# Optimization experiments

Hardware: AMD Instinct MI355X
Metric: run time of the kernel (lower is better)

The kernel has to match this reference:

```python
import jax, jax.numpy as jnp
import numpy as np

B, T, D, H = 64, 512, 1024, 1024


def setup_inputs() -> dict:
    key = jax.random.key(0)
    ks = jax.random.split(key, 8)
    s_in = 1.0 / np.sqrt(D).astype(np.float32)
    s_h = 1.0 / np.sqrt(H).astype(np.float32)
    return {
        "x": jax.random.normal(ks[0], (B, T, D), jnp.float32),
        "lengths": jax.random.randint(ks[1], (B,), 0, T),
        "k0": jax.random.normal(ks[2], (D, 3 * H), jnp.float32) * s_in,
        "rk0": jax.random.normal(ks[3], (H, 3 * H), jnp.float32) * s_h,
        "b0": jax.random.normal(ks[4], (2, 3 * H), jnp.float32) * 0.02,
        "k1": jax.random.normal(ks[5], (H, 3 * H), jnp.float32) * s_h,
        "rk1": jax.random.normal(ks[6], (H, 3 * H), jnp.float32) * s_h,
        "b1": jax.random.normal(ks[7], (2, 3 * H), jnp.float32) * 0.02,
    }


def _gru_step(h, xt, k, rk, b):
    # Keras GRUCell, reset_after=True (v2): separate input/recurrent biases.
    mx = xt @ k + b[0]          # [B, 3H]
    mh = h @ rk + b[1]          # [B, 3H]
    xz, xr, xh = jnp.split(mx, 3, axis=-1)
    hz, hr, hh = jnp.split(mh, 3, axis=-1)
    z = jax.nn.sigmoid(xz + hz)
    r = jax.nn.sigmoid(xr + hr)
    cand = jnp.tanh(xh + r * hh)
    return z * h + (1.0 - z) * cand


def reference(x, lengths, k0, rk0, b0, k1, rk1, b1):
    Bb, Tt, _ = x.shape
    mask = jnp.arange(Tt)[None, :] < lengths[:, None]   # [B, T]

    def step(carry, inp):
        h0, h1 = carry
        xt, mt = inp                                    # xt [B,D], mt [B]
        nh0 = _gru_step(h0, xt, k0, rk0, b0)
        nh1 = _gru_step(h1, nh0, k1, rk1, b1)
        m = mt[:, None]
        h0 = jnp.where(m, nh0, h0)                      # masked steps carry state
        h1 = jnp.where(m, nh1, h1)
        return (h0, h1), h1                             # output = top-layer state

    h_init = (jnp.zeros((Bb, k1.shape[1] // 3), x.dtype),
              jnp.zeros((Bb, k1.shape[1] // 3), x.dtype))
    _, ys = jax.lax.scan(step, h_init, (x.transpose(1, 0, 2), mask.T))
    return ys.transpose(1, 0, 2)                        # [B, T, H]
```

## Files before the change

kernel.cpp:

```cpp
#include <hip/hip_runtime.h>
#include <cstdint>


typedef unsigned short u16;
typedef __bf16 bf16x8 __attribute__((ext_vector_type(8)));
typedef float f32x4 __attribute__((ext_vector_type(4)));

#define B_   64
#define T_   512
#define D_   1024
#define H_   1024
#define N3_  3072
#define TC_  32
#define NCH_ 16
#define MROWS_ (B_ * TC_)

#define MFMA(a, b, c) __builtin_amdgcn_mfma_f32_16x16x32_bf16((a), (b), (c), 0, 0, 0)

static __device__ __forceinline__ u16 f2bf(float x) {
  unsigned u = __float_as_uint(x);
  u += 0x7FFFu + ((u >> 16) & 1u);
  return (u16)(u >> 16);
}
static __device__ __forceinline__ float bf2f(u16 s) {
  return __uint_as_float(((unsigned)s) << 16);
}

__global__ void init_ws(u16* s0h, u16* s0l, u16* s1h, u16* s1l,
                        unsigned* bars) {
  int i = blockIdx.x * blockDim.x + threadIdx.x;
  if (i < B_ * H_) { s0h[i] = 0; s0l[i] = 0; s1h[i] = 0; s1l[i] = 0; }
  if (i < 2 * NCH_ * 256) bars[i] = 0;
}

__global__ void split_x_chunk(const float* __restrict__ x, int t0,
                              u16* __restrict__ hi, u16* __restrict__ lo) {
  int i = blockIdx.x * blockDim.x + threadIdx.x;
  int m = i >> 8;
  int c = i & 255;
  int tl = m >> 6;
  int b = m & 63;
  float4 v = ((const float4*)x)[((size_t)b * T_ + t0 + tl) * 256 + c];
  u16 h0 = f2bf(v.x), h1 = f2bf(v.y), h2 = f2bf(v.z), h3 = f2bf(v.w);
  u16 g0 = f2bf(v.x - bf2f(h0)), g1 = f2bf(v.y - bf2f(h1));
  u16 g2 = f2bf(v.z - bf2f(h2)), g3 = f2bf(v.w - bf2f(h3));
  uint2 ph, pl;
  ph.x = (unsigned)h0 | ((unsigned)h1 << 16);
  ph.y = (unsigned)h2 | ((unsigned)h3 << 16);
  pl.x = (unsigned)g0 | ((unsigned)g1 << 16);
  pl.y = (unsigned)g2 | ((unsigned)g3 << 16);
  *(uint2*)(hi + (size_t)i * 4) = ph;
  *(uint2*)(lo + (size_t)i * 4) = pl;
}

__global__ void transpose_split(const float* __restrict__ src, u16* __restrict__ dhi,
                                u16* __restrict__ dlo) {
  __shared__ float tile[32][33];
  const int tx = threadIdx.x, ty = threadIdx.y;
  const int n0 = blockIdx.x * 32, k0 = blockIdx.y * 32;
  #pragma unroll
  for (int i = 0; i < 4; ++i)
    tile[ty + 8 * i][tx] = src[(size_t)(k0 + ty + 8 * i) * N3_ + n0 + tx];
  __syncthreads();
  #pragma unroll
  for (int i = 0; i < 4; ++i) {
    float v = tile[tx][ty + 8 * i];
    size_t o = (size_t)(n0 + ty + 8 * i) * 1024 + k0 + tx;
    u16 h = f2bf(v);
    dhi[o] = h;
    dlo[o] = f2bf(v - bf2f(h));
  }
}

__global__ __launch_bounds__(256, 1) void gemm_bf16x3(
    const u16* __restrict__ Ahi, const u16* __restrict__ Alo,
    const u16* __restrict__ Bhi, const u16* __restrict__ Blo,
    const float* __restrict__ bias, float* __restrict__ C) {
  __shared__ u16 lds[4 * 128 * 64];
  u16* ldsAh = lds;
  u16* ldsAl = lds + 128 * 64;
  u16* ldsBh = lds + 2 * 128 * 64;
  u16* ldsBl = lds + 3 * 128 * 64;

  const int tid = threadIdx.x;
  const int wave = tid >> 6, lane = tid & 63;
  const int l15 = lane & 15, l4 = lane >> 4;
  const int wm = wave >> 1, wn = wave & 1;
  const int m0 = blockIdx.y * 128, n0 = blockIdx.x * 128;

  f32x4 acc[4][4];
  f32x4 zero = {0.f, 0.f, 0.f, 0.f};
  #pragma unroll
  for (int i = 0; i < 4; ++i)
    #pragma unroll
    for (int j = 0; j < 4; ++j) acc[i][j] = zero;

  for (int kt = 0; kt < 16; ++kt) {
    #pragma unroll
    for (int q = 0; q < 4; ++q) {
      int chunk = q * 256 + tid;
      int row = chunk >> 3, cc = chunk & 7;
      int sc = cc ^ (row & 7);
      size_t ga = (size_t)(m0 + row) * 1024 + kt * 64 + cc * 8;
      size_t gb = (size_t)(n0 + row) * 1024 + kt * 64 + cc * 8;
      int lo_ = row * 64 + sc * 8;
      *(uint4*)(ldsAh + lo_) = *(const uint4*)(Ahi + ga);
      *(uint4*)(ldsAl + lo_) = *(const uint4*)(Alo + ga);
      *(uint4*)(ldsBh + lo_) = *(const uint4*)(Bhi + gb);
      *(uint4*)(ldsBl + lo_) = *(const uint4*)(Blo + gb);
    }
    __syncthreads();
    #pragma unroll
    for (int kk = 0; kk < 2; ++kk) {
      bf16x8 ah[4], al[4], bh[4], bl[4];
      #pragma unroll
      for (int mt = 0; mt < 4; ++mt) {
        int row = wm * 64 + mt * 16 + l15;
        int off = row * 64 + ((4 * kk + l4) ^ (row & 7)) * 8;
        ah[mt] = *(const bf16x8*)(ldsAh + off);
        al[mt] = *(const bf16x8*)(ldsAl + off);
      }
      #pragma unroll
      for (int nt = 0; nt < 4; ++nt) {
        int row = wn * 64 + nt * 16 + l15;
        int off = row * 64 + ((4 * kk + l4) ^ (row & 7)) * 8;
        bh[nt] = *(const bf16x8*)(ldsBh + off);
        bl[nt] = *(const bf16x8*)(ldsBl + off);
      }
      #pragma unroll
      for (int mt = 0; mt < 4; ++mt)
        #pragma unroll
        for (int nt = 0; nt < 4; ++nt) {
          acc[mt][nt] = MFMA(ah[mt], bh[nt], acc[mt][nt]);
          acc[mt][nt] = MFMA(ah[mt], bl[nt], acc[mt][nt]);
          acc[mt][nt] = MFMA(al[mt], bh[nt], acc[mt][nt]);
        }
    }
    __syncthreads();
  }
  #pragma unroll
  for (int nt = 0; nt < 4; ++nt) {
    int col = n0 + wn * 64 + nt * 16 + l15;
    float bv = bias[col];
    #pragma unroll
    for (int mt = 0; mt < 4; ++mt) {
      int rowb = m0 + wm * 64 + mt * 16 + 4 * l4;
      #pragma unroll
      for (int r = 0; r < 4; ++r)
        C[(size_t)(rowb + r) * N3_ + col] = acc[mt][nt][r] + bv;
    }
  }
}

__global__ __launch_bounds__(256, 1) void gru_rec_v2(
    const float* __restrict__ mx, const u16* __restrict__ wTh,
    const u16* __restrict__ wTl, const float* __restrict__ bias,
    const int* __restrict__ lengths, u16* __restrict__ Sh, u16* __restrict__ Sl,
    u16* __restrict__ Hh, u16* __restrict__ Hl, float* __restrict__ outF32,
    unsigned* __restrict__ bars, int t0) {
  __shared__ __align__(16) char lds[77824];
  char* ldsAh = lds;
  char* ldsAl = lds + 32768;
  char* ldsRed = lds + 65536;

  const int bid = blockIdx.x;
  const int colgrp = bid & 63, mtile = bid >> 6;
  const int tid = threadIdx.x;
  const int wave = tid >> 6, lane = tid & 63;
  const int l15 = lane & 15, l4 = lane >> 4;
  const int ccol = colgrp * 16 + l15;
  unsigned* bar = bars + mtile * 64;

  const int kbase = wave * 256 + 8 * l4;
  bf16x8 Wh[3][8], Wl[3][8];
  #pragma unroll
  for (int g = 0; g < 3; ++g) {
    const size_t wrow = ((size_t)(g * 1024 + ccol)) * 1024 + kbase;
    #pragma unroll
    for (int ks = 0; ks < 8; ++ks) {
      Wh[g][ks] = *(const bf16x8*)(wTh + wrow + ks * 32);
      Wl[g][ks] = *(const bf16x8*)(wTl + wrow + ks * 32);
    }
  }

  const float bz = bias[ccol], br = bias[1024 + ccol], bh = bias[2048 + ccol];
  const int brow = mtile * 16 + 4 * l4;
  int lens[4];
  #pragma unroll
  for (int r = 0; r < 4; ++r) lens[r] = lengths[brow + r];
  const int grow0 = mtile * 16;

  #pragma unroll 1
  for (int tl = 0; tl < TC_; ++tl) {
    const u16* srcH = (tl == 0) ? Sh : (Hh + (size_t)(tl - 1) * B_ * H_);
    const u16* srcL = (tl == 0) ? Sl : (Hl + (size_t)(tl - 1) * B_ * H_);

    float pxz[4], pxr[4], pxh[4], phold[4];
    if (wave == 0) {
      #pragma unroll
      for (int r = 0; r < 4; ++r) {
        int b = brow + r;
        size_t mrow = ((size_t)tl * B_ + b) * N3_;
        pxz[r] = mx[mrow + ccol];
        pxr[r] = mx[mrow + 1024 + ccol];
        pxh[r] = mx[mrow + 2048 + ccol];
        size_t poff = (size_t)b * H_ + ccol;
        phold[r] = bf2f(srcH[poff]) + bf2f(srcL[poff]);
      }
    }

    #pragma unroll
    for (int i = 0; i < 8; ++i) {
      int c = i * 256 + tid;
      int row = c >> 7, k16 = c & 127;
      int dso = row * 2048 + ((k16 * 16) ^ ((row & 7) << 4));
      size_t go = (size_t)(grow0 + row) * H_ + k16 * 8;
      *(uint4*)(ldsAh + dso) = *(const uint4*)(srcH + go);
      *(uint4*)(ldsAl + dso) = *(const uint4*)(srcL + go);
    }
    __syncthreads();

    f32x4 a0 = {0.f, 0.f, 0.f, 0.f};
    f32x4 a1 = a0, a2 = a0;
    #pragma unroll
    for (int ks = 0; ks < 8; ++ks) {
      int k16 = wave * 32 + ks * 4 + l4;
      int dso = l15 * 2048 + ((k16 * 16) ^ ((l15 & 7) << 4));
      bf16x8 ah = *(const bf16x8*)(ldsAh + dso);
      bf16x8 al = *(const bf16x8*)(ldsAl + dso);
      a0 = MFMA(ah, Wh[0][ks], a0); a0 = MFMA(ah, Wl[0][ks], a0); a0 = MFMA(al, Wh[0][ks], a0);
      a1 = MFMA(ah, Wh[1][ks], a1); a1 = MFMA(ah, Wl[1][ks], a1); a1 = MFMA(al, Wh[1][ks], a1);
      a2 = MFMA(ah, Wh[2][ks], a2); a2 = MFMA(ah, Wl[2][ks], a2); a2 = MFMA(al, Wh[2][ks], a2);
    }

    if (wave != 0) {
      int rb = (wave - 1) * 3072;
      *(f32x4*)(ldsRed + rb + 0 * 1024 + lane * 16) = a0;
      *(f32x4*)(ldsRed + rb + 1 * 1024 + lane * 16) = a1;
      *(f32x4*)(ldsRed + rb + 2 * 1024 + lane * 16) = a2;
    }
    __syncthreads();

    if (wave == 0) {
      #pragma unroll
      for (int w = 1; w < 4; ++w) {
        int rb = (w - 1) * 3072;
        a0 += *(const f32x4*)(ldsRed + rb + 0 * 1024 + lane * 16);
        a1 += *(const f32x4*)(ldsRed + rb + 1 * 1024 + lane * 16);
        a2 += *(const f32x4*)(ldsRed + rb + 2 * 1024 + lane * 16);
      }
      const int t = t0 + tl;
      #pragma unroll
      for (int r = 0; r < 4; ++r) {
        int b = brow + r;
        float hz = a0[r] + bz, hr = a1[r] + br, hhv = a2[r] + bh;
        float z  = 1.f / (1.f + __expf(-(pxz[r] + hz)));
        float rg = 1.f / (1.f + __expf(-(pxr[r] + hr)));
        float ct = pxh[r] + rg * hhv;
        float e2 = __expf(2.f * ct);
        float cand = 1.f - 2.f / (e2 + 1.f);
        float hnew = (t < lens[r]) ? (z * phold[r] + (1.f - z) * cand) : phold[r];
        size_t crow = ((size_t)tl * B_ + b) * H_ + ccol;
        u16 nhi = f2bf(hnew);
        u16 nlo = f2bf(hnew - bf2f(nhi));
        Hh[crow] = nhi; Hl[crow] = nlo;
        if (outF32) outF32[((size_t)b * T_ + t) * H_ + ccol] = hnew;
        if (tl == TC_ - 1) {
          size_t poff = (size_t)b * H_ + ccol;
          Sh[poff] = nhi; Sl[poff] = nlo;
        }
      }
    }

    if (tl != TC_ - 1) {
      if (tid == 0) {
        __hip_atomic_fetch_add(bar, 1u, __ATOMIC_RELEASE, __HIP_MEMORY_SCOPE_AGENT);
        unsigned tgt = 64u * (unsigned)(tl + 1);
        while (__hip_atomic_load(bar, __ATOMIC_RELAXED, __HIP_MEMORY_SCOPE_AGENT) < tgt)
          __builtin_amdgcn_s_sleep(8);
        __threadfence();
      }
      __syncthreads();
    }
  }
}

extern "C" void kernel_launch(void* const* d_in, const int* in_sizes, int n_in,
                              void* d_out, int out_size, void* d_ws, size_t ws_size,
                              hipStream_t stream) {
  (void)in_sizes; (void)n_in; (void)out_size; (void)ws_size;
  const float* x      = (const float*)d_in[0];
  const int* lengths  = (const int*)d_in[1];
  const float* k0     = (const float*)d_in[2];
  const float* rk0    = (const float*)d_in[3];
  const float* b0     = (const float*)d_in[4];
  const float* k1     = (const float*)d_in[5];
  const float* rk1    = (const float*)d_in[6];
  const float* b1     = (const float*)d_in[7];
  float* out = (float*)d_out;
  char* ws = (char*)d_ws;

  const size_t WB = (size_t)N3_ * 1024 * 2;
  const size_t XB = (size_t)MROWS_ * 1024 * 2;
  size_t off = 0;
  u16* k0Th  = (u16*)(ws + off); off += WB;
  u16* k0Tl  = (u16*)(ws + off); off += WB;
  u16* rk0Th = (u16*)(ws + off); off += WB;
  u16* rk0Tl = (u16*)(ws + off); off += WB;
  u16* k1Th  = (u16*)(ws + off); off += WB;
  u16* k1Tl  = (u16*)(ws + off); off += WB;
  u16* rk1Th = (u16*)(ws + off); off += WB;
  u16* rk1Tl = (u16*)(ws + off); off += WB;
  u16* XCh   = (u16*)(ws + off); off += XB;
  u16* XCl   = (u16*)(ws + off); off += XB;
  float* MX  = (float*)(ws + off); off += (size_t)MROWS_ * N3_ * 4;
  u16* H0h   = (u16*)(ws + off); off += XB;
  u16* H0l   = (u16*)(ws + off); off += XB;
  u16* H1h   = (u16*)(ws + off); off += XB;
  u16* H1l   = (u16*)(ws + off); off += XB;
  u16* S0h   = (u16*)(ws + off); off += (size_t)B_ * H_ * 2;
  u16* S0l   = (u16*)(ws + off); off += (size_t)B_ * H_ * 2;
  u16* S1h   = (u16*)(ws + off); off += (size_t)B_ * H_ * 2;
  u16* S1l   = (u16*)(ws + off); off += (size_t)B_ * H_ * 2;
  unsigned* bars = (unsigned*)(ws + off); off += (size_t)2 * NCH_ * 256 * 4;

  init_ws<<<256, 256, 0, stream>>>(S0h, S0l, S1h, S1l, bars);

  dim3 tb(32, 8), tg(96, 32);
  transpose_split<<<tg, tb, 0, stream>>>(k0,  k0Th,  k0Tl);
  transpose_split<<<tg, tb, 0, stream>>>(rk0, rk0Th, rk0Tl);
  transpose_split<<<tg, tb, 0, stream>>>(k1,  k1Th,  k1Tl);
  transpose_split<<<tg, tb, 0, stream>>>(rk1, rk1Th, rk1Tl);

  for (int c = 0; c < NCH_; ++c) {
    int t0 = c * TC_;
    split_x_chunk<<<2048, 256, 0, stream>>>(x, t0, XCh, XCl);
    gemm_bf16x3<<<dim3(24, 16), 256, 0, stream>>>(XCh, XCl, k0Th, k0Tl, b0, MX);
    gru_rec_v2<<<256, 256, 0, stream>>>(MX, rk0Th, rk0Tl, b0 + N3_, lengths,
                                        S0h, S0l, H0h, H0l, nullptr,
                                        bars + (size_t)c * 256, t0);
    gemm_bf16x3<<<dim3(24, 16), 256, 0, stream>>>(H0h, H0l, k1Th, k1Tl, b1, MX);
    gru_rec_v2<<<256, 256, 0, stream>>>(MX, rk1Th, rk1Tl, b1 + N3_, lengths,
                                        S1h, S1l, H1h, H1l, out,
                                        bars + (size_t)(NCH_ + c) * 256, t0);
  }
}
```

Measured before the change: 15.47 ms.

## Pack hidden state hi/lo into u32 and lighten cross-block barrier

```diff
diff --git a/kernel.cpp b/kernel.cpp
--- a/kernel.cpp
+++ b/kernel.cpp
@@ -3,6 +3,8 @@
 
 
 typedef unsigned short u16;
+typedef unsigned int u32;
+typedef unsigned long long u64;
 typedef __bf16 bf16x8 __attribute__((ext_vector_type(8)));
 typedef float f32x4 __attribute__((ext_vector_type(4)));
 
@@ -26,10 +28,9 @@
   return __uint_as_float(((unsigned)s) << 16);
 }
 
-__global__ void init_ws(u16* s0h, u16* s0l, u16* s1h, u16* s1l,
-                        unsigned* bars) {
+__global__ void init_ws(u32* s0, u32* s1, unsigned* bars) {
   int i = blockIdx.x * blockDim.x + threadIdx.x;
-  if (i < B_ * H_) { s0h[i] = 0; s0l[i] = 0; s1h[i] = 0; s1l[i] = 0; }
+  if (i < B_ * H_) { s0[i] = 0; s1[i] = 0; }
   if (i < 2 * NCH_ * 256) bars[i] = 0;
 }
 
@@ -152,15 +153,15 @@
   }
 }
 
-__global__ __launch_bounds__(256, 1) void gru_rec_v2(
+__global__ __launch_bounds__(256, 1) void gru_rec_v3(
     const float* __restrict__ mx, const u16* __restrict__ wTh,
     const u16* __restrict__ wTl, const float* __restrict__ bias,
-    const int* __restrict__ lengths, u16* __restrict__ Sh, u16* __restrict__ Sl,
+    const int* __restrict__ lengths,
+    u32* __restrict__ Spk, u32* __restrict__ Hpk,
     u16* __restrict__ Hh, u16* __restrict__ Hl, float* __restrict__ outF32,
     unsigned* __restrict__ bars, int t0) {
-  __shared__ __align__(16) char lds[77824];
-  char* ldsAh = lds;
-  char* ldsAl = lds + 32768;
+  __shared__ __align__(16) char lds[74752];
+  char* ldsP = lds;
   char* ldsRed = lds + 65536;
 
   const int bid = blockIdx.x;
@@ -170,6 +171,7 @@
   const int l15 = lane & 15, l4 = lane >> 4;
   const int ccol = colgrp * 16 + l15;
   unsigned* bar = bars + mtile * 64;
+  const int grow0 = mtile * 16;
 
   const int kbase = wave * 256 + 8 * l4;
   bf16x8 Wh[3][8], Wl[3][8];
@@ -188,12 +190,10 @@
   int lens[4];
   #pragma unroll
   for (int r = 0; r < 4; ++r) lens[r] = lengths[brow + r];
-  const int grow0 = mtile * 16;
 
   #pragma unroll 1
   for (int tl = 0; tl < TC_; ++tl) {
-    const u16* srcH = (tl == 0) ? Sh : (Hh + (size_t)(tl - 1) * B_ * H_);
-    const u16* srcL = (tl == 0) ? Sl : (Hl + (size_t)(tl - 1) * B_ * H_);
+    const u32* srcPk = (tl == 0) ? Spk : (Hpk + (size_t)(tl - 1) * B_ * H_);
 
     float pxz[4], pxr[4], pxh[4], phold[4];
     if (wave == 0) {
@@ -204,33 +204,44 @@
         pxz[r] = mx[mrow + ccol];
         pxr[r] = mx[mrow + 1024 + ccol];
         pxh[r] = mx[mrow + 2048 + ccol];
-        size_t poff = (size_t)b * H_ + ccol;
-        phold[r] = bf2f(srcH[poff]) + bf2f(srcL[poff]);
-      }
-    }
-
-    #pragma unroll
-    for (int i = 0; i < 8; ++i) {
-      int c = i * 256 + tid;
-      int row = c >> 7, k16 = c & 127;
-      int dso = row * 2048 + ((k16 * 16) ^ ((row & 7) << 4));
-      size_t go = (size_t)(grow0 + row) * H_ + k16 * 8;
-      *(uint4*)(ldsAh + dso) = *(const uint4*)(srcH + go);
-      *(uint4*)(ldsAl + dso) = *(const uint4*)(srcL + go);
+        u32 p = __hip_atomic_load((u32*)(srcPk + (size_t)b * H_ + ccol),
+                                  __ATOMIC_RELAXED, __HIP_MEMORY_SCOPE_AGENT);
+        phold[r] = bf2f((u16)(p >> 16)) + bf2f((u16)(p & 0xFFFFu));
+      }
+    }
+
+    #pragma unroll
+    for (int i = 0; i < 32; ++i) {
+      int o = (i * 256 + tid) * 8;
+      int row = o >> 12;
+      int cb = o & 4095;
+      u64 v = __hip_atomic_load(
+          (u64*)(srcPk + (size_t)(grow0 + row) * H_ + (cb >> 2)),
+          __ATOMIC_RELAXED, __HIP_MEMORY_SCOPE_AGENT);
+      *(u64*)(ldsP + row * 4096 + (cb ^ ((row & 7) << 4))) = v;
     }
     __syncthreads();
 
     f32x4 a0 = {0.f, 0.f, 0.f, 0.f};
     f32x4 a1 = a0, a2 = a0;
+    const int rbase = l15 * 4096;
+    const int sw = (l15 & 7) << 4;
     #pragma unroll
     for (int ks = 0; ks < 8; ++ks) {
-      int k16 = wave * 32 + ks * 4 + l4;
-      int dso = l15 * 2048 + ((k16 * 16) ^ ((l15 & 7) << 4));
-      bf16x8 ah = *(const bf16x8*)(ldsAh + dso);
-      bf16x8 al = *(const bf16x8*)(ldsAl + dso);
-      a0 = MFMA(ah, Wh[0][ks], a0); a0 = MFMA(ah, Wl[0][ks], a0); a0 = MFMA(al, Wh[0][ks], a0);
-      a1 = MFMA(ah, Wh[1][ks], a1); a1 = MFMA(ah, Wl[1][ks], a1); a1 = MFMA(al, Wh[1][ks], a1);
-      a2 = MFMA(ah, Wh[2][ks], a2); a2 = MFMA(ah, Wl[2][ks], a2); a2 = MFMA(al, Wh[2][ks], a2);
+      int bo = (wave * 32 + ks * 4 + l4) * 32;
+      uint4 pA = *(const uint4*)(ldsP + rbase + (bo ^ sw));
+      uint4 pB = *(const uint4*)(ldsP + rbase + ((bo + 16) ^ sw));
+      u32 c0_[8] = {pA.x, pA.y, pA.z, pA.w, pB.x, pB.y, pB.z, pB.w};
+      union { u32 u[4]; bf16x8 v; } ah, al;
+      #pragma unroll
+      for (int j = 0; j < 4; ++j) {
+        u32 c0 = c0_[2 * j], c1 = c0_[2 * j + 1];
+        ah.u[j] = (c0 >> 16) | (c1 & 0xFFFF0000u);
+        al.u[j] = (c0 & 0xFFFFu) | (c1 << 16);
+      }
+      a0 = MFMA(ah.v, Wh[0][ks], a0); a0 = MFMA(ah.v, Wl[0][ks], a0); a0 = MFMA(al.v, Wh[0][ks], a0);
+      a1 = MFMA(ah.v, Wh[1][ks], a1); a1 = MFMA(ah.v, Wl[1][ks], a1); a1 = MFMA(al.v, Wh[1][ks], a1);
+      a2 = MFMA(ah.v, Wh[2][ks], a2); a2 = MFMA(ah.v, Wl[2][ks], a2); a2 = MFMA(al.v, Wh[2][ks], a2);
     }
 
     if (wave != 0) {
@@ -260,25 +271,25 @@
         float e2 = __expf(2.f * ct);
         float cand = 1.f - 2.f / (e2 + 1.f);
         float hnew = (t < lens[r]) ? (z * phold[r] + (1.f - z) * cand) : phold[r];
-        size_t crow = ((size_t)tl * B_ + b) * H_ + ccol;
         u16 nhi = f2bf(hnew);
         u16 nlo = f2bf(hnew - bf2f(nhi));
-        Hh[crow] = nhi; Hl[crow] = nlo;
+        u32 pk = ((u32)nhi << 16) | nlo;
+        size_t crow = ((size_t)tl * B_ + b) * H_ + ccol;
+        if (Hh) { Hh[crow] = nhi; Hl[crow] = nlo; }
+        __hip_atomic_store(Hpk + (size_t)tl * B_ * H_ + (size_t)b * H_ + ccol,
+                           pk, __ATOMIC_RELAXED, __HIP_MEMORY_SCOPE_AGENT);
         if (outF32) outF32[((size_t)b * T_ + t) * H_ + ccol] = hnew;
-        if (tl == TC_ - 1) {
-          size_t poff = (size_t)b * H_ + ccol;
-          Sh[poff] = nhi; Sl[poff] = nlo;
-        }
+        if (tl == TC_ - 1) Spk[(size_t)b * H_ + ccol] = pk;
       }
     }
 
     if (tl != TC_ - 1) {
       if (tid == 0) {
-        __hip_atomic_fetch_add(bar, 1u, __ATOMIC_RELEASE, __HIP_MEMORY_SCOPE_AGENT);
+        asm volatile("s_waitcnt vmcnt(0)" ::: "memory");
+        __hip_atomic_fetch_add(bar, 1u, __ATOMIC_RELAXED, __HIP_MEMORY_SCOPE_AGENT);
         unsigned tgt = 64u * (unsigned)(tl + 1);
         while (__hip_atomic_load(bar, __ATOMIC_RELAXED, __HIP_MEMORY_SCOPE_AGENT) < tgt)
-          __builtin_amdgcn_s_sleep(8);
-        __threadfence();
+          __builtin_amdgcn_s_sleep(1);
       }
       __syncthreads();
     }
@@ -316,15 +327,12 @@
   float* MX  = (float*)(ws + off); off += (size_t)MROWS_ * N3_ * 4;
   u16* H0h   = (u16*)(ws + off); off += XB;
   u16* H0l   = (u16*)(ws + off); off += XB;
-  u16* H1h   = (u16*)(ws + off); off += XB;
-  u16* H1l   = (u16*)(ws + off); off += XB;
-  u16* S0h   = (u16*)(ws + off); off += (size_t)B_ * H_ * 2;
-  u16* S0l   = (u16*)(ws + off); off += (size_t)B_ * H_ * 2;
-  u16* S1h   = (u16*)(ws + off); off += (size_t)B_ * H_ * 2;
-  u16* S1l   = (u16*)(ws + off); off += (size_t)B_ * H_ * 2;
+  u32* Spk0  = (u32*)(ws + off); off += (size_t)B_ * H_ * 4;
+  u32* Spk1  = (u32*)(ws + off); off += (size_t)B_ * H_ * 4;
   unsigned* bars = (unsigned*)(ws + off); off += (size_t)2 * NCH_ * 256 * 4;
-
-  init_ws<<<256, 256, 0, stream>>>(S0h, S0l, S1h, S1l, bars);
+  u32* Hpk = (u32*)XCh;
+
+  init_ws<<<256, 256, 0, stream>>>(Spk0, Spk1, bars);
 
   dim3 tb(32, 8), tg(96, 32);
   transpose_split<<<tg, tb, 0, stream>>>(k0,  k0Th,  k0Tl);
@@ -336,12 +344,12 @@
     int t0 = c * TC_;
     split_x_chunk<<<2048, 256, 0, stream>>>(x, t0, XCh, XCl);
     gemm_bf16x3<<<dim3(24, 16), 256, 0, stream>>>(XCh, XCl, k0Th, k0Tl, b0, MX);
-    gru_rec_v2<<<256, 256, 0, stream>>>(MX, rk0Th, rk0Tl, b0 + N3_, lengths,
-                                        S0h, S0l, H0h, H0l, nullptr,
+    gru_rec_v3<<<256, 256, 0, stream>>>(MX, rk0Th, rk0Tl, b0 + N3_, lengths,
+                                        Spk0, Hpk, H0h, H0l, nullptr,
                                         bars + (size_t)c * 256, t0);
     gemm_bf16x3<<<dim3(24, 16), 256, 0, stream>>>(H0h, H0l, k1Th, k1Tl, b1, MX);
-    gru_rec_v2<<<256, 256, 0, stream>>>(MX, rk1Th, rk1Tl, b1 + N3_, lengths,
-                                        S1h, S1l, H1h, H1l, out,
+    gru_rec_v3<<<256, 256, 0, stream>>>(MX, rk1Th, rk1Tl, b1 + N3_, lengths,
+                                        Spk1, Hpk, (u16*)nullptr, (u16*)nullptr, out,
                                         bars + (size_t)(NCH_ + c) * 256, t0);
   }
 }
```

After: 14.16 ms. 1.09x faster.
